# Kernel tuning notes

Measured on AMD Instinct MI355X. Metric: run time of the kernel, lower is better.

## Reference

```python
import jax, jax.numpy as jnp
import numpy as np

N, E, G = 50000, 800000, 1024
IN, HID, H, L = 128, 128, 4, 3
C = HID // H  # per-head channels = 32
NEG_SLOPE = 0.2
BN_EPS = 1e-5


def setup_inputs() -> dict:
    key = jax.random.key(0)
    ks = jax.random.split(key, 12)
    s = 0.05
    x = jax.random.normal(ks[0], (N, IN), dtype=jnp.float32)
    edge_index = jax.random.randint(ks[1], (2, E), 0, N, dtype=jnp.int32)
    batch = jnp.sort(jax.random.randint(ks[2], (N,), 0, G, dtype=jnp.int32))
    # GATConv params per layer (in_dim == hidden_dim so all layers stack)
    Ws = jax.random.normal(ks[3], (L, HID, HID), dtype=jnp.float32) * s
    att_src = jax.random.normal(ks[4], (L, H, C), dtype=jnp.float32) * s
    att_dst = jax.random.normal(ks[5], (L, H, C), dtype=jnp.float32) * s
    biases = jax.random.normal(ks[6], (L, HID), dtype=jnp.float32) * s
    gammas = jnp.ones((L, HID), dtype=jnp.float32)
    betas = jnp.zeros((L, HID), dtype=jnp.float32)
    lin1_w = jax.random.normal(ks[7], (HID, HID // 2), dtype=jnp.float32) * s
    lin1_b = jnp.zeros((HID // 2,), dtype=jnp.float32)
    lin2_w = jax.random.normal(ks[8], (HID // 2, 1), dtype=jnp.float32) * s
    lin2_b = jnp.zeros((1,), dtype=jnp.float32)
    return dict(x=x, edge_index=edge_index, batch=batch, Ws=Ws, att_src=att_src,
                att_dst=att_dst, biases=biases, gammas=gammas, betas=betas,
                lin1_w=lin1_w, lin1_b=lin1_b, lin2_w=lin2_w, lin2_b=lin2_b)


def _gat_layer(x, src, dst, W, a_src, a_dst, bias):
    h = (x @ W).reshape(N, H, C)                      # [N,H,C]
    e_src = jnp.einsum('nhc,hc->nh', h, a_src)        # [N,H]
    e_dst = jnp.einsum('nhc,hc->nh', h, a_dst)
    e = jax.nn.leaky_relu(e_src[src] + e_dst[dst], NEG_SLOPE)  # [E',H]
    m = jax.ops.segment_max(e, dst, num_segments=N)   # segment softmax over dst
    ex = jnp.exp(e - m[dst])
    den = jax.ops.segment_sum(ex, dst, num_segments=N)
    alpha = ex / (den[dst] + 1e-16)
    msg = h[src] * alpha[:, :, None]                  # [E',H,C]
    out = jax.ops.segment_sum(msg, dst, num_segments=N).reshape(N, HID)
    return out + bias


def reference(x, edge_index, batch, Ws, att_src, att_dst, biases, gammas, betas,
              lin1_w, lin1_b, lin2_w, lin2_b):
    loop = jnp.arange(N, dtype=edge_index.dtype)      # add_self_loops=True
    src = jnp.concatenate([edge_index[0], loop])
    dst = jnp.concatenate([edge_index[1], loop])
    for l in range(L):
        h = _gat_layer(x, src, dst, Ws[l], att_src[l], att_dst[l], biases[l])
        mean = h.mean(axis=0)                         # BatchNorm1d (batch stats)
        var = h.var(axis=0)
        h = (h - mean) / jnp.sqrt(var + BN_EPS) * gammas[l] + betas[l]
        x = jax.nn.elu(h)
    cnt = jax.ops.segment_sum(jnp.ones((N,), x.dtype), batch, num_segments=G)
    pooled = jax.ops.segment_sum(x, batch, num_segments=G) / jnp.maximum(cnt, 1.0)[:, None]
    h1 = jax.nn.relu(pooled @ lin1_w + lin1_b)
    return (h1 @ lin2_w + lin2_b)[:, 0]               # [G]
```

## Files before the change

### kernel.cpp

```cpp
#include <hip/hip_runtime.h>
#include <hip/hip_fp16.h>
#include <math.h>

#define NN 50000
#define EE 800000
#define GG 1024
#define HIDD 128
#define NHEAD 4
#define EPTOT (EE + NN)
#define NEG_SLOPE 0.2f
#define NB ((NN + 255) / 256)
#define NTILE (NN / 16)

#define BSHIFT 9
#define NBUK 98
#define PCHUNK 4096
#define BCAP 10240

typedef _Float16 f16x8 __attribute__((ext_vector_type(8)));
typedef float f32x4 __attribute__((ext_vector_type(4)));

__global__ void zero_kernel(float* __restrict__ p, int n) {
  int i = blockIdx.x * blockDim.x + threadIdx.x;
  if (i < n) p[i] = 0.f;
}

__global__ void count_kernel(const int* __restrict__ ei, int* __restrict__ deg) {
  int e = blockIdx.x * blockDim.x + threadIdx.x;
  if (e >= EPTOT) return;
  int d = (e < EE) ? ei[EE + e] : (e - EE);
  atomicAdd(&deg[d], 1);
}

__global__ __launch_bounds__(256) void degsum_kernel(const int* __restrict__ deg,
                                                     int* __restrict__ bsum) {
  __shared__ int sh[256];
  int i = blockIdx.x * 256 + threadIdx.x;
  sh[threadIdx.x] = (i < NN) ? deg[i] : 0;
  __syncthreads();
  for (int off = 128; off > 0; off >>= 1) {
    if (threadIdx.x < off) sh[threadIdx.x] += sh[threadIdx.x + off];
    __syncthreads();
  }
  if (threadIdx.x == 0) bsum[blockIdx.x] = sh[0];
}

__global__ __launch_bounds__(256) void scanb_kernel(const int* __restrict__ bsum,
                                                    int* __restrict__ boff,
                                                    int* __restrict__ rowptr) {
  __shared__ int sh[256];
  int t = threadIdx.x;
  int v = (t < NB) ? bsum[t] : 0;
  sh[t] = v;
  __syncthreads();
  for (int off = 1; off < 256; off <<= 1) {
    int u = (t >= off) ? sh[t - off] : 0;
    __syncthreads();
    sh[t] += u;
    __syncthreads();
  }
  if (t < NB) boff[t] = sh[t] - v;
  if (t == 255) rowptr[NN] = sh[255];
}

__global__ __launch_bounds__(256) void rowptr_kernel(const int* __restrict__ deg,
                                                     const int* __restrict__ boff,
                                                     int* __restrict__ rowptr) {
  __shared__ int sh[256];
  int t = threadIdx.x;
  int i = blockIdx.x * 256 + t;
  int v = (i < NN) ? deg[i] : 0;
  sh[t] = v;
  __syncthreads();
  for (int off = 1; off < 256; off <<= 1) {
    int u = (t >= off) ? sh[t - off] : 0;
    __syncthreads();
    sh[t] += u;
    __syncthreads();
  }
  if (i < NN) rowptr[i] = boff[blockIdx.x] + sh[t] - v;
}

__global__ void bcurinit_kernel(const int* __restrict__ rowptr, int* __restrict__ bcur) {
  int b = threadIdx.x;
  if (b < NBUK) bcur[b] = rowptr[b << BSHIFT];
}

__global__ __launch_bounds__(256) void partA_kernel(const int* __restrict__ ei,
                                                    int* __restrict__ bcur,
                                                    unsigned long long* __restrict__ pairs) {
  __shared__ int hist[NBUK];
  __shared__ int sbase[NBUK];
  int t = threadIdx.x;
  if (t < NBUK) hist[t] = 0;
  __syncthreads();
  int e0 = blockIdx.x * PCHUNK;
  int ss[16], dd[16];
  int cnt = 0;
#pragma unroll
  for (int i = 0; i < 16; ++i) {
    int e = e0 + i * 256 + t;
    if (e < EPTOT) {
      int s, d;
      if (e < EE) { s = ei[e]; d = ei[EE + e]; } else { s = e - EE; d = s; }
      ss[cnt] = s; dd[cnt] = d; ++cnt;
      atomicAdd(&hist[d >> BSHIFT], 1);
    }
  }
  __syncthreads();
  if (t < NBUK) {
    int h = hist[t];
    sbase[t] = h ? atomicAdd(&bcur[t], h) : 0;
    hist[t] = 0;
  }
  __syncthreads();
  for (int i = 0; i < cnt; ++i) {
    int b = dd[i] >> BSHIFT;
    int pos = sbase[b] + atomicAdd(&hist[b], 1);
    pairs[pos] = ((unsigned long long)(unsigned)dd[i] << 32) | (unsigned)ss[i];
  }
}

__global__ __launch_bounds__(512) void partB_kernel(const unsigned long long* __restrict__ pairs,
                                                    const int* __restrict__ rowptr,
                                                    int* __restrict__ colb) {
  __shared__ int cur[512];
  __shared__ int stage[BCAP];
  int b = blockIdx.x;
  int t = threadIdx.x;
  int node0 = b << BSHIFT;
  int node1 = min(node0 + 512, NN);
  int base = rowptr[node0];
  int nE = rowptr[node1] - base;
  cur[t] = (node0 + t < node1) ? (rowptr[node0 + t] - base) : 0;
  __syncthreads();
  for (int j = t; j < nE; j += 512) {
    unsigned long long p = pairs[base + j];
    int d = (int)(p >> 32);
    int s = (int)(p & 0xffffffffu);
    int pl = atomicAdd(&cur[d - node0], 1);
    if (pl < BCAP) stage[pl] = s;
    else colb[base + pl] = s;
  }
  __syncthreads();
  int lim = min(nE, BCAP);
  for (int j = t; j < lim; j += 512) colb[base + j] = stage[j];
}

__device__ inline float bnelu1(float v, float scale, float shift) {
  v = v * scale + shift;
  return (v > 0.f) ? v : expm1f(v);
}

__global__ __launch_bounds__(256) void prepack_kernel(const float* __restrict__ Ws,
                                                      _Float16* __restrict__ Wp) {
  int f = blockIdx.x * 256 + threadIdx.x;
  if (f >= 3 * 2048) return;
  int layer = f >> 11, r = f & 2047;
  int ctile = r >> 8, ks = (r >> 6) & 3, lane = r & 63;
  const float* W = Ws + (size_t)layer * HIDD * HIDD;
  int col = ctile * 16 + (lane & 15);
  int krow = ks * 32 + (lane >> 4) * 8;
  f16x8 v;
#pragma unroll
  for (int j = 0; j < 8; ++j) v[j] = (_Float16)W[(krow + j) * HIDD + col];
  *(f16x8*)(Wp + (size_t)f * 8) = v;
}

__global__ void bnfinal_kernel(const float* __restrict__ stat,
                               const float* __restrict__ gamma,
                               const float* __restrict__ beta,
                               float* __restrict__ scsh) {
  int c = threadIdx.x;
  const float invN = 1.f / (float)NN;
  float mean = stat[c] * invN;
  float var = stat[128 + c] * invN - mean * mean;
  float scale = gamma[c] * rsqrtf(var + 1e-5f);
  scsh[c] = scale;
  scsh[128 + c] = beta[c] - mean * scale;
}

__global__ __launch_bounds__(256) void gemm_mfma_kernel(
    const float* __restrict__ X, const _Float16* __restrict__ Wp,
    const float* __restrict__ scsh, const float* __restrict__ asrc,
    const float* __restrict__ adst, __half* __restrict__ Hh,
    float* __restrict__ esrc, float* __restrict__ edst) {
  int wave = threadIdx.x >> 6, lane = threadIdx.x & 63;
  int jt = blockIdx.x * 4 + wave;
  if (jt >= NTILE) return;
  int nl = lane & 15, kg = lane >> 4;
  int node = jt * 16 + nl;
  const float* xrow = X + (size_t)node * HIDD;
  f32x4 acc[8];
#pragma unroll
  for (int c = 0; c < 8; ++c) acc[c] = (f32x4){0.f, 0.f, 0.f, 0.f};
#pragma unroll
  for (int ks = 0; ks < 4; ++ks) {
    int k0 = ks * 32 + kg * 8;
    float4 va = *(const float4*)(xrow + k0);
    float4 vb = *(const float4*)(xrow + k0 + 4);
    if (scsh) {
      float4 s0 = *(const float4*)(scsh + k0);
      float4 s1 = *(const float4*)(scsh + k0 + 4);
      float4 t0 = *(const float4*)(scsh + HIDD + k0);
      float4 t1 = *(const float4*)(scsh + HIDD + k0 + 4);
      va.x = bnelu1(va.x, s0.x, t0.x); va.y = bnelu1(va.y, s0.y, t0.y);
      va.z = bnelu1(va.z, s0.z, t0.z); va.w = bnelu1(va.w, s0.w, t0.w);
      vb.x = bnelu1(vb.x, s1.x, t1.x); vb.y = bnelu1(vb.y, s1.y, t1.y);
      vb.z = bnelu1(vb.z, s1.z, t1.z); vb.w = bnelu1(vb.w, s1.w, t1.w);
    }
    f16x8 bfrag;
    bfrag[0] = (_Float16)va.x; bfrag[1] = (_Float16)va.y;
    bfrag[2] = (_Float16)va.z; bfrag[3] = (_Float16)va.w;
    bfrag[4] = (_Float16)vb.x; bfrag[5] = (_Float16)vb.y;
    bfrag[6] = (_Float16)vb.z; bfrag[7] = (_Float16)vb.w;
#pragma unroll
    for (int c = 0; c < 8; ++c) {
      f16x8 afrag = *(const f16x8*)(Wp + (((size_t)(c * 4 + ks) * 64 + lane) << 3));
      acc[c] = __builtin_amdgcn_mfma_f32_16x16x32_f16(afrag, bfrag, acc[c], 0, 0, 0);
    }
  }
  float es_p[4] = {0.f, 0.f, 0.f, 0.f};
  float ed_p[4] = {0.f, 0.f, 0.f, 0.f};
  __half* hrow = Hh + (size_t)node * HIDD;
#pragma unroll
  for (int c = 0; c < 8; ++c) {
    int ch0 = c * 16 + kg * 4;
    __half2 h01 = __floats2half2_rn(acc[c][0], acc[c][1]);
    __half2 h23 = __floats2half2_rn(acc[c][2], acc[c][3]);
    union { __half2 h[2]; float2 f; } u;
    u.h[0] = h01; u.h[1] = h23;
    *(float2*)(hrow + ch0) = u.f;
    float4 av = *(const float4*)(asrc + ch0);
    float4 bv = *(const float4*)(adst + ch0);
    int hd = c >> 1;
    es_p[hd] += acc[c][0] * av.x + acc[c][1] * av.y + acc[c][2] * av.z + acc[c][3] * av.w;
    ed_p[hd] += acc[c][0] * bv.x + acc[c][1] * bv.y + acc[c][2] * bv.z + acc[c][3] * bv.w;
  }
#pragma unroll
  for (int hd = 0; hd < 4; ++hd) {
    es_p[hd] += __shfl_xor(es_p[hd], 16);
    es_p[hd] += __shfl_xor(es_p[hd], 32);
    ed_p[hd] += __shfl_xor(ed_p[hd], 16);
    ed_p[hd] += __shfl_xor(ed_p[hd], 32);
  }
  float es_o = (kg == 0) ? es_p[0] : (kg == 1) ? es_p[1] : (kg == 2) ? es_p[2] : es_p[3];
  float ed_o = (kg == 0) ? ed_p[0] : (kg == 1) ? ed_p[1] : (kg == 2) ? ed_p[2] : ed_p[3];
  esrc[node * 4 + kg] = es_o;
  edst[node * 4 + kg] = ed_o;
}

__global__ __launch_bounds__(256) void agg_kernel(const __half2* __restrict__ Hh,
                                                  const float* __restrict__ esrc,
                                                  const float* __restrict__ edst,
                                                  const int* __restrict__ rowptr,
                                                  const int* __restrict__ colb,
                                                  const float* __restrict__ bias,
                                                  float* __restrict__ out) {
  int wid = (blockIdx.x * 256 + threadIdx.x) >> 6;
  int lane = threadIdx.x & 63;
  if (wid >= NN) return;
  int hd = lane >> 4;
  float ed = edst[wid * 4 + hd];
  int e0 = rowptr[wid], e1 = rowptr[wid + 1];
  float den = 0.f, ax = 0.f, ay = 0.f;
  const __half2* hbase = Hh + lane;
  int src = colb[e0];
  float es = esrc[src * 4 + hd];
  __half2 hv = hbase[(size_t)src * 64];
  for (int e = e0; e < e1; ++e) {
    int srcn = (e + 1 < e1) ? colb[e + 1] : src;
    float esn = esrc[srcn * 4 + hd];
    __half2 hvn = hbase[(size_t)srcn * 64];
    float z = es + ed;
    z = (z > 0.f) ? z : NEG_SLOPE * z;
    float w = __expf(z);
    float2 f = __half22float2(hv);
    den += w;
    ax += w * f.x;
    ay += w * f.y;
    src = srcn; es = esn; hv = hvn;
  }
  float inv = 1.f / (den + 1e-16f);
  int c = 2 * lane;
  out[(size_t)wid * HIDD + c] = ax * inv + bias[c];
  out[(size_t)wid * HIDD + c + 1] = ay * inv + bias[c + 1];
}

__global__ __launch_bounds__(256) void bnstat_kernel(const float* __restrict__ X,
                                                     float* __restrict__ stat) {
  __shared__ float sh[256];
  int tid = threadIdx.x;
  int c = tid & 127;
  int half = tid >> 7;
  float s = 0.f, q = 0.f;
  for (int r = blockIdx.x * 2 + half; r < NN; r += gridDim.x * 2) {
    float v = X[(size_t)r * HIDD + c];
    s += v;
    q += v * v;
  }
  sh[tid] = s;
  __syncthreads();
  if (tid < 128) atomicAdd(&stat[c], s + sh[tid + 128]);
  __syncthreads();
  sh[tid] = q;
  __syncthreads();
  if (tid < 128) atomicAdd(&stat[128 + c], q + sh[tid + 128]);
}

__global__ void gbound_kernel(const int* __restrict__ batch, int* __restrict__ gstart) {
  int i = blockIdx.x * blockDim.x + threadIdx.x;
  if (i >= NN) return;
  int cur = batch[i];
  int prev = (i == 0) ? -1 : batch[i - 1];
  for (int g = prev + 1; g <= cur; ++g) gstart[g] = i;
  if (i == NN - 1) {
    for (int g = cur + 1; g <= GG; ++g) gstart[g] = NN;
  }
}

__global__ __launch_bounds__(128) void pool_kernel(const float* __restrict__ X,
                                                   const int* __restrict__ gstart,
                                                   const float* __restrict__ scsh,
                                                   float* __restrict__ pooled) {
  int g = blockIdx.x;
  int c = threadIdx.x;
  float scale = scsh[c];
  float shift = scsh[128 + c];
  int n0 = gstart[g], n1 = gstart[g + 1];
  float s = 0.f;
  for (int n = n0; n < n1; ++n) s += bnelu1(X[(size_t)n * HIDD + c], scale, shift);
  float inv = (n1 > n0) ? 1.f / (float)(n1 - n0) : 0.f;
  pooled[(size_t)g * HIDD + c] = s * inv;
}

__global__ __launch_bounds__(256) void head_kernel(const float* __restrict__ pooled,
                                                   const float* __restrict__ w1,
                                                   const float* __restrict__ b1,
                                                   const float* __restrict__ w2,
                                                   const float* __restrict__ b2,
                                                   float* __restrict__ out) {
  int wid = (blockIdx.x * 256 + threadIdx.x) >> 6;
  int lane = threadIdx.x & 63;
  if (wid >= GG) return;
  float acc = b1[lane];
  const float* pg = pooled + (size_t)wid * HIDD;
  for (int k = 0; k < HIDD; ++k) {
    acc += pg[k] * w1[k * 64 + lane];
  }
  acc = fmaxf(acc, 0.f);
  float v = acc * w2[lane];
#pragma unroll
  for (int off = 32; off > 0; off >>= 1) v += __shfl_down(v, off);
  if (lane == 0) out[wid] = v + b2[0];
}

extern "C" void kernel_launch(void* const* d_in, const int* in_sizes, int n_in,
                              void* d_out, int out_size, void* d_ws, size_t ws_size,
                              hipStream_t stream) {
  const float* x    = (const float*)d_in[0];
  const int* ei     = (const int*)d_in[1];
  const int* batch  = (const int*)d_in[2];
  const float* Ws   = (const float*)d_in[3];
  const float* asrc = (const float*)d_in[4];
  const float* adst = (const float*)d_in[5];
  const float* bias = (const float*)d_in[6];
  const float* gam  = (const float*)d_in[7];
  const float* bet  = (const float*)d_in[8];
  const float* w1   = (const float*)d_in[9];
  const float* b1   = (const float*)d_in[10];
  const float* w2   = (const float*)d_in[11];
  const float* b2   = (const float*)d_in[12];
  float* out = (float*)d_out;

  char* wp = (char*)d_ws;
  auto carve = [&](size_t bytes) -> char* {
    char* p = wp;
    wp += (bytes + 255) & ~(size_t)255;
    return p;
  };
  float* B      = (float*)carve((size_t)NN * HIDD * 4);
  __half* Hh    = (__half*)carve((size_t)NN * HIDD * 2);
  _Float16* Wp  = (_Float16*)carve((size_t)3 * HIDD * HIDD * 2);
  float* scsh   = (float*)carve((size_t)3 * 256 * 4);
  float* esrc   = (float*)carve((size_t)NN * NHEAD * 4);
  float* edst   = (float*)carve((size_t)NN * NHEAD * 4);
  int* rowptr   = (int*)carve((size_t)(NN + 1) * 4);
  int* colb     = (int*)carve((size_t)EPTOT * 4);
  unsigned long long* pairs = (unsigned long long*)carve((size_t)EPTOT * 8);
  int* bcur     = (int*)carve((size_t)NBUK * 4);
  int* bsum     = (int*)carve((size_t)NB * 4);
  int* boff     = (int*)carve((size_t)NB * 4);
  int* gstart   = (int*)carve((size_t)(GG + 1) * 4);
  float* pooled = (float*)carve((size_t)GG * HIDD * 4);
  char* z0 = wp;
  int* deg      = (int*)carve((size_t)NN * 4);
  float* stats  = (float*)carve(768 * 4);
  int zcount = (int)((wp - z0) / 4);

  zero_kernel<<<(zcount + 255) / 256, 256, 0, stream>>>((float*)z0, zcount);
  prepack_kernel<<<24, 256, 0, stream>>>(Ws, Wp);
  count_kernel<<<(EPTOT + 255) / 256, 256, 0, stream>>>(ei, deg);
  degsum_kernel<<<NB, 256, 0, stream>>>(deg, bsum);
  scanb_kernel<<<1, 256, 0, stream>>>(bsum, boff, rowptr);
  rowptr_kernel<<<NB, 256, 0, stream>>>(deg, boff, rowptr);
  bcurinit_kernel<<<1, 128, 0, stream>>>(rowptr, bcur);
  partA_kernel<<<(EPTOT + PCHUNK - 1) / PCHUNK, 256, 0, stream>>>(ei, bcur, pairs);
  partB_kernel<<<NBUK, 512, 0, stream>>>(pairs, rowptr, colb);
  gbound_kernel<<<(NN + 255) / 256, 256, 0, stream>>>(batch, gstart);

  const float* xin = x;
  for (int l = 0; l < 3; ++l) {
    const float* sc_prev = (l == 0) ? nullptr : scsh + (l - 1) * 256;
    gemm_mfma_kernel<<<(NTILE + 3) / 4, 256, 0, stream>>>(
        xin, Wp + (size_t)l * HIDD * HIDD, sc_prev,
        asrc + l * NHEAD * 32, adst + l * NHEAD * 32, Hh, esrc, edst);
    agg_kernel<<<(NN * 64 + 255) / 256, 256, 0, stream>>>(
        (const __half2*)Hh, esrc, edst, rowptr, colb, bias + l * HIDD, B);
    bnstat_kernel<<<256, 256, 0, stream>>>(B, stats + l * 256);
    bnfinal_kernel<<<1, 128, 0, stream>>>(stats + l * 256, gam + l * HIDD,
                                          bet + l * HIDD, scsh + l * 256);
    xin = B;
  }
  pool_kernel<<<GG, 128, 0, stream>>>(B, gstart, scsh + 2 * 256, pooled);
  head_kernel<<<(GG * 64 + 255) / 256, 256, 0, stream>>>(pooled, w1, b1, w2, b2, out);
}
```

Before: 450.5 us.

## Store aggregated layer output in fp16 and batch gather loads in aggregation

The per-layer aggregation output buffer changes from fp32 to fp16, and the GEMM, BN-stat and pooling kernels read half-precision input, so the intermediate traffic is halved. The aggregation loop is restructured to issue four independent neighbour gathers per iteration instead of a one-ahead software prefetch, aiming to expose more memory-level parallelism. The BN-stat grid grows from 256 to 1024 blocks. The cost is extra rounding of pre-BatchNorm activations to fp16, which may affect accuracy.

```diff
diff --git a/kernel.cpp b/kernel.cpp
--- a/kernel.cpp
+++ b/kernel.cpp
@@ -181,39 +181,49 @@
 }
 
 __global__ __launch_bounds__(256) void gemm_mfma_kernel(
-    const float* __restrict__ X, const _Float16* __restrict__ Wp,
-    const float* __restrict__ scsh, const float* __restrict__ asrc,
-    const float* __restrict__ adst, __half* __restrict__ Hh,
-    float* __restrict__ esrc, float* __restrict__ edst) {
+    const float* __restrict__ Xf, const __half* __restrict__ Xh,
+    const _Float16* __restrict__ Wp, const float* __restrict__ scsh,
+    const float* __restrict__ asrc, const float* __restrict__ adst,
+    __half* __restrict__ Hh, float* __restrict__ esrc, float* __restrict__ edst) {
   int wave = threadIdx.x >> 6, lane = threadIdx.x & 63;
   int jt = blockIdx.x * 4 + wave;
   if (jt >= NTILE) return;
   int nl = lane & 15, kg = lane >> 4;
   int node = jt * 16 + nl;
-  const float* xrow = X + (size_t)node * HIDD;
   f32x4 acc[8];
 #pragma unroll
   for (int c = 0; c < 8; ++c) acc[c] = (f32x4){0.f, 0.f, 0.f, 0.f};
 #pragma unroll
   for (int ks = 0; ks < 4; ++ks) {
     int k0 = ks * 32 + kg * 8;
-    float4 va = *(const float4*)(xrow + k0);
-    float4 vb = *(const float4*)(xrow + k0 + 4);
-    if (scsh) {
+    f16x8 bfrag;
+    if (Xf) {
+      const float* xrow = Xf + (size_t)node * HIDD;
+      float4 va = *(const float4*)(xrow + k0);
+      float4 vb = *(const float4*)(xrow + k0 + 4);
+      bfrag[0] = (_Float16)va.x; bfrag[1] = (_Float16)va.y;
+      bfrag[2] = (_Float16)va.z; bfrag[3] = (_Float16)va.w;
+      bfrag[4] = (_Float16)vb.x; bfrag[5] = (_Float16)vb.y;
+      bfrag[6] = (_Float16)vb.z; bfrag[7] = (_Float16)vb.w;
+    } else {
+      const __half2* xrow = (const __half2*)(Xh + (size_t)node * HIDD + k0);
       float4 s0 = *(const float4*)(scsh + k0);
       float4 s1 = *(const float4*)(scsh + k0 + 4);
       float4 t0 = *(const float4*)(scsh + HIDD + k0);
       float4 t1 = *(const float4*)(scsh + HIDD + k0 + 4);
-      va.x = bnelu1(va.x, s0.x, t0.x); va.y = bnelu1(va.y, s0.y, t0.y);
-      va.z = bnelu1(va.z, s0.z, t0.z); va.w = bnelu1(va.w, s0.w, t0.w);
-      vb.x = bnelu1(vb.x, s1.x, t1.x); vb.y = bnelu1(vb.y, s1.y, t1.y);
-      vb.z = bnelu1(vb.z, s1.z, t1.z); vb.w = bnelu1(vb.w, s1.w, t1.w);
+      float2 f0 = __half22float2(xrow[0]);
+      float2 f1 = __half22float2(xrow[1]);
+      float2 f2 = __half22float2(xrow[2]);
+      float2 f3 = __half22float2(xrow[3]);
+      bfrag[0] = (_Float16)bnelu1(f0.x, s0.x, t0.x);
+      bfrag[1] = (_Float16)bnelu1(f0.y, s0.y, t0.y);
+      bfrag[2] = (_Float16)bnelu1(f1.x, s0.z, t0.z);
+      bfrag[3] = (_Float16)bnelu1(f1.y, s0.w, t0.w);
+      bfrag[4] = (_Float16)bnelu1(f2.x, s1.x, t1.x);
+      bfrag[5] = (_Float16)bnelu1(f2.y, s1.y, t1.y);
+      bfrag[6] = (_Float16)bnelu1(f3.x, s1.z, t1.z);
+      bfrag[7] = (_Float16)bnelu1(f3.y, s1.w, t1.w);
     }
-    f16x8 bfrag;
-    bfrag[0] = (_Float16)va.x; bfrag[1] = (_Float16)va.y;
-    bfrag[2] = (_Float16)va.z; bfrag[3] = (_Float16)va.w;
-    bfrag[4] = (_Float16)vb.x; bfrag[5] = (_Float16)vb.y;
-    bfrag[6] = (_Float16)vb.z; bfrag[7] = (_Float16)vb.w;
 #pragma unroll
     for (int c = 0; c < 8; ++c) {
       f16x8 afrag = *(const f16x8*)(Wp + (((size_t)(c * 4 + ks) * 64 + lane) << 3));
@@ -256,7 +266,7 @@
                                                   const int* __restrict__ rowptr,
                                                   const int* __restrict__ colb,
                                                   const float* __restrict__ bias,
-                                                  float* __restrict__ out) {
+                                                  __half* __restrict__ outh) {
   int wid = (blockIdx.x * 256 + threadIdx.x) >> 6;
   int lane = threadIdx.x & 63;
   if (wid >= NN) return;
@@ -265,29 +275,49 @@
   int e0 = rowptr[wid], e1 = rowptr[wid + 1];
   float den = 0.f, ax = 0.f, ay = 0.f;
   const __half2* hbase = Hh + lane;
-  int src = colb[e0];
-  float es = esrc[src * 4 + hd];
-  __half2 hv = hbase[(size_t)src * 64];
-  for (int e = e0; e < e1; ++e) {
-    int srcn = (e + 1 < e1) ? colb[e + 1] : src;
-    float esn = esrc[srcn * 4 + hd];
-    __half2 hvn = hbase[(size_t)srcn * 64];
-    float z = es + ed;
-    z = (z > 0.f) ? z : NEG_SLOPE * z;
+  int e = e0;
+  for (; e + 4 <= e1; e += 4) {
+    int s[4];
+#pragma unroll
+    for (int j = 0; j < 4; ++j) s[j] = colb[e + j];
+    float es[4];
+    __half2 hv[4];
+#pragma unroll
+    for (int j = 0; j < 4; ++j) {
+      es[j] = esrc[s[j] * 4 + hd];
+      hv[j] = hbase[(size_t)s[j] * 64];
+    }
+#pragma unroll
+    for (int j = 0; j < 4; ++j) {
+      float z = es[j] + ed;
+      z = fmaxf(z, NEG_SLOPE * z);
+      float w = __expf(z);
+      float2 f = __half22float2(hv[j]);
+      den += w;
+      ax += w * f.x;
+      ay += w * f.y;
+    }
+  }
+  for (; e < e1; ++e) {
+    int src = colb[e];
+    float esv = esrc[src * 4 + hd];
+    __half2 hvv = hbase[(size_t)src * 64];
+    float z = esv + ed;
+    z = fmaxf(z, NEG_SLOPE * z);
     float w = __expf(z);
-    float2 f = __half22float2(hv);
+    float2 f = __half22float2(hvv);
     den += w;
     ax += w * f.x;
     ay += w * f.y;
-    src = srcn; es = esn; hv = hvn;
   }
   float inv = 1.f / (den + 1e-16f);
   int c = 2 * lane;
-  out[(size_t)wid * HIDD + c] = ax * inv + bias[c];
-  out[(size_t)wid * HIDD + c + 1] = ay * inv + bias[c + 1];
-}
-
-__global__ __launch_bounds__(256) void bnstat_kernel(const float* __restrict__ X,
+  float vx = ax * inv + bias[c];
+  float vy = ay * inv + bias[c + 1];
+  *((__half2*)(outh + (size_t)wid * HIDD) + lane) = __floats2half2_rn(vx, vy);
+}
+
+__global__ __launch_bounds__(256) void bnstat_kernel(const __half* __restrict__ X,
                                                      float* __restrict__ stat) {
   __shared__ float sh[256];
   int tid = threadIdx.x;
@@ -295,7 +325,7 @@
   int half = tid >> 7;
   float s = 0.f, q = 0.f;
   for (int r = blockIdx.x * 2 + half; r < NN; r += gridDim.x * 2) {
-    float v = X[(size_t)r * HIDD + c];
+    float v = __half2float(X[(size_t)r * HIDD + c]);
     s += v;
     q += v * v;
   }
@@ -319,7 +349,7 @@
   }
 }
 
-__global__ __launch_bounds__(128) void pool_kernel(const float* __restrict__ X,
+__global__ __launch_bounds__(128) void pool_kernel(const __half* __restrict__ X,
                                                    const int* __restrict__ gstart,
                                                    const float* __restrict__ scsh,
                                                    float* __restrict__ pooled) {
@@ -329,7 +359,8 @@
   float shift = scsh[128 + c];
   int n0 = gstart[g], n1 = gstart[g + 1];
   float s = 0.f;
-  for (int n = n0; n < n1; ++n) s += bnelu1(X[(size_t)n * HIDD + c], scale, shift);
+  for (int n = n0; n < n1; ++n)
+    s += bnelu1(__half2float(X[(size_t)n * HIDD + c]), scale, shift);
   float inv = (n1 > n0) ? 1.f / (float)(n1 - n0) : 0.f;
   pooled[(size_t)g * HIDD + c] = s * inv;
 }
@@ -379,7 +410,7 @@
     wp += (bytes + 255) & ~(size_t)255;
     return p;
   };
-  float* B      = (float*)carve((size_t)NN * HIDD * 4);
+  __half* B     = (__half*)carve((size_t)NN * HIDD * 2);
   __half* Hh    = (__half*)carve((size_t)NN * HIDD * 2);
   _Float16* Wp  = (_Float16*)carve((size_t)3 * HIDD * HIDD * 2);
   float* scsh   = (float*)carve((size_t)3 * 256 * 4);
@@ -409,18 +440,18 @@
   partB_kernel<<<NBUK, 512, 0, stream>>>(pairs, rowptr, colb);
   gbound_kernel<<<(NN + 255) / 256, 256, 0, stream>>>(batch, gstart);
 
-  const float* xin = x;
   for (int l = 0; l < 3; ++l) {
     const float* sc_prev = (l == 0) ? nullptr : scsh + (l - 1) * 256;
+    const float* xf = (l == 0) ? x : nullptr;
+    const __half* xh = (l == 0) ? nullptr : B;
     gemm_mfma_kernel<<<(NTILE + 3) / 4, 256, 0, stream>>>(
-        xin, Wp + (size_t)l * HIDD * HIDD, sc_prev,
+        xf, xh, Wp + (size_t)l * HIDD * HIDD, sc_prev,
         asrc + l * NHEAD * 32, adst + l * NHEAD * 32, Hh, esrc, edst);
     agg_kernel<<<(NN * 64 + 255) / 256, 256, 0, stream>>>(
         (const __half2*)Hh, esrc, edst, rowptr, colb, bias + l * HIDD, B);
-    bnstat_kernel<<<256, 256, 0, stream>>>(B, stats + l * 256);
+    bnstat_kernel<<<1024, 256, 0, stream>>>(B, stats + l * 256);
     bnfinal_kernel<<<1, 128, 0, stream>>>(stats + l * 256, gam + l * HIDD,
                                           bet + l * HIDD, scsh + l * 256);
-    xin = B;
   }
   pool_kernel<<<GG, 128, 0, stream>>>(B, gstart, scsh + 2 * 256, pooled);
   head_kernel<<<(GG * 64 + 255) / 256, 256, 0, stream>>>(pooled, w1, b1, w2, b2, out);
```

After: 407.0 us. 9.7% less time.
